# Kernel optimization log

Hardware: AMD Instinct MI355X
Metric: run time of the kernel (lower is better)

The kernel has to match this reference:

```python
import jax, jax.numpy as jnp
import numpy as np

N_NODES = 50000


def setup_inputs() -> dict:
    key = jax.random.key(0)
    k1, k2, k3, k4, k5, k6 = jax.random.split(key, 6)
    N, T, F_IN, F_OUT, E = N_NODES, 4, 64, 64, 800000
    node_features = jax.random.normal(k1, (N, T, F_IN), dtype=jnp.float32)
    edge_weights = jax.random.uniform(k2, (T, E), dtype=jnp.float32)
    src = jax.random.randint(k3, (E,), 0, N, dtype=jnp.int32)
    dst = jax.random.randint(k4, (E,), 0, N, dtype=jnp.int32)
    weight = jax.random.normal(k5, (F_OUT, F_IN), dtype=jnp.float32) / np.sqrt(F_IN)
    bias = jax.random.normal(k6, (F_OUT,), dtype=jnp.float32) * 0.01
    return {"node_features": node_features, "edge_weights": edge_weights,
            "src": src, "dst": dst, "weight": weight, "bias": bias}


def reference(node_features, edge_weights, src, dst, weight, bias):
    # edge_weights: (T, E) -> per-edge weights (E, T)
    ew = edge_weights.T  # (E, T)
    # gather source node features: (E, T, F); multiply by per-edge/timestep scalar
    msg = ew[:, :, None] * node_features[src]  # (E, T, F)
    # scatter-sum into destination nodes: (N, T, F)
    h = jax.ops.segment_sum(msg, dst, num_segments=N_NODES)
    # final linear: (N, T, F_out)
    out = jnp.einsum('ntf,of->nto', h, weight) + bias
    return out
```

## Files before the change

### kernel.cpp

```cpp
#include <hip/hip_runtime.h>


#define F_DIM 64
#define TF 256

typedef __attribute__((ext_vector_type(8))) short bf16x8;
typedef __attribute__((ext_vector_type(4))) float f32x4;
union frag_u { bf16x8 v; unsigned short s[8]; };

__device__ __forceinline__ unsigned short f2bf(float x) {
  unsigned u = __float_as_uint(x);
  return (unsigned short)((u + 0x7FFF + ((u >> 16) & 1)) >> 16);
}
__device__ __forceinline__ float bf2f(unsigned short b) {
  return __uint_as_float(((unsigned)b) << 16);
}

__global__ __launch_bounds__(256) void transform_hist_kernel(
    const float4* __restrict__ nf4, const float* __restrict__ W,
    unsigned short* __restrict__ nfb, int nrows,
    const int* __restrict__ dst, int* __restrict__ cnt, int E) {
  int lane = threadIdx.x & 63;
  int l15 = lane & 15, lg = lane >> 4;
  int wid = (blockIdx.x * 256 + threadIdx.x) >> 6;
  int nw = (gridDim.x * 256) >> 6;

  frag_u a[4][2];
  #pragma unroll
  for (int ot = 0; ot < 4; ++ot) {
    #pragma unroll
    for (int kh = 0; kh < 2; ++kh) {
      const float* wp = W + (ot * 16 + l15) * 64 + kh * 32 + lg * 8;
      float4 v0 = *reinterpret_cast<const float4*>(wp);
      float4 v1 = *reinterpret_cast<const float4*>(wp + 4);
      a[ot][kh].s[0] = f2bf(v0.x); a[ot][kh].s[1] = f2bf(v0.y);
      a[ot][kh].s[2] = f2bf(v0.z); a[ot][kh].s[3] = f2bf(v0.w);
      a[ot][kh].s[4] = f2bf(v1.x); a[ot][kh].s[5] = f2bf(v1.y);
      a[ot][kh].s[6] = f2bf(v1.z); a[ot][kh].s[7] = f2bf(v1.w);
    }
  }

  int ntiles = (nrows + 15) >> 4;
  for (int tile = wid; tile < ntiles; tile += nw) {
    int r = tile * 16 + l15;
    int rc = min(r, nrows - 1);
    const float4* bp = nf4 + (size_t)rc * 16 + lg * 2;
    float4 v0 = bp[0], v1 = bp[1];
    float4 v2 = bp[8], v3 = bp[9];
    frag_u b0, b1;
    b0.s[0] = f2bf(v0.x); b0.s[1] = f2bf(v0.y);
    b0.s[2] = f2bf(v0.z); b0.s[3] = f2bf(v0.w);
    b0.s[4] = f2bf(v1.x); b0.s[5] = f2bf(v1.y);
    b0.s[6] = f2bf(v1.z); b0.s[7] = f2bf(v1.w);
    b1.s[0] = f2bf(v2.x); b1.s[1] = f2bf(v2.y);
    b1.s[2] = f2bf(v2.z); b1.s[3] = f2bf(v2.w);
    b1.s[4] = f2bf(v3.x); b1.s[5] = f2bf(v3.y);
    b1.s[6] = f2bf(v3.z); b1.s[7] = f2bf(v3.w);

    f32x4 acc[4];
    #pragma unroll
    for (int ot = 0; ot < 4; ++ot) {
      f32x4 z = {0.f, 0.f, 0.f, 0.f};
      acc[ot] = __builtin_amdgcn_mfma_f32_16x16x32_bf16(a[ot][0].v, b0.v, z, 0, 0, 0);
      acc[ot] = __builtin_amdgcn_mfma_f32_16x16x32_bf16(a[ot][1].v, b1.v, acc[ot], 0, 0, 0);
    }
    if (r < nrows) {
      #pragma unroll
      for (int ot = 0; ot < 4; ++ot) {
        ushort4 u = make_ushort4(f2bf(acc[ot][0]), f2bf(acc[ot][1]),
                                 f2bf(acc[ot][2]), f2bf(acc[ot][3]));
        *reinterpret_cast<ushort4*>(
            &nfb[(size_t)r * F_DIM + ot * 16 + lg * 4]) = u;
      }
    }
  }

  int gtid = blockIdx.x * 256 + threadIdx.x;
  int gsz = gridDim.x * 256;
  for (int e = gtid; e < E; e += gsz) atomicAdd(&cnt[dst[e]], 1);
}

__global__ __launch_bounds__(1024) void scan_kernel(
    const int* __restrict__ cnt, int* __restrict__ off, int* __restrict__ bsum,
    int* __restrict__ sync, int N) {
  __shared__ int wsum[16];
  __shared__ int isLast;
  int tid = threadIdx.x;
  if (tid == 0) isLast = 0;
  int i = blockIdx.x * 1024 + tid;
  int v = (i < N) ? cnt[i] : 0;
  int lane = tid & 63;
  int incl = v;
  #pragma unroll
  for (int s = 1; s < 64; s <<= 1) {
    int t = __shfl_up(incl, s, 64);
    if (lane >= s) incl += t;
  }
  int w = tid >> 6;
  if (lane == 63) wsum[w] = incl;
  __syncthreads();
  if (w == 0) {
    int x = (lane < 16) ? wsum[lane] : 0;
    #pragma unroll
    for (int s = 1; s < 16; s <<= 1) {
      int t = __shfl_up(x, s, 64);
      if (lane >= s) x += t;
    }
    if (lane < 16) wsum[lane] = x;
  }
  __syncthreads();
  int wpre = (w == 0) ? 0 : wsum[w - 1];
  if (i < N) off[i] = wpre + incl - v;

  if (tid == 1023) {
    atomicExch(&bsum[blockIdx.x], wpre + incl);
    __threadfence();
    if (atomicAdd(sync, 1) == (int)gridDim.x - 1) isLast = 1;
  }
  __syncthreads();
  if (isLast && tid < 64) {
    int nb = gridDim.x;
    int bv = (tid < nb) ? atomicAdd(&bsum[tid], 0) : 0;
    int binc = bv;
    #pragma unroll
    for (int s = 1; s < 64; s <<= 1) {
      int t = __shfl_up(binc, s, 64);
      if (lane >= s) binc += t;
    }
    if (tid < nb) atomicExch(&bsum[tid], binc - bv);
  }
}

__global__ __launch_bounds__(256) void fill_kernel(
    const int* __restrict__ dst, const int* __restrict__ src,
    const float* __restrict__ ew, const int* __restrict__ off,
    const int* __restrict__ bsum, int* __restrict__ cnt,
    uint4* __restrict__ rec, int E) {
  int e = blockIdx.x * 256 + threadIdx.x;
  if (e < E) {
    int d = dst[e];
    int pos = off[d] + bsum[d >> 10] + atomicSub(&cnt[d], 1) - 1;
    unsigned w0 = f2bf(ew[e]),         w1 = f2bf(ew[E + e]);
    unsigned w2 = f2bf(ew[2 * E + e]), w3 = f2bf(ew[3 * E + e]);
    uint4 r;
    r.x = (unsigned)src[e];
    r.y = (w1 << 16) | w0;
    r.z = (w3 << 16) | w2;
    r.w = 0;
    rec[pos] = r;
  }
}

__global__ __launch_bounds__(256) void gather_bf16_kernel(
    const ushort4* __restrict__ nfb, const uint4* __restrict__ rec,
    const int* __restrict__ off, const int* __restrict__ bsum,
    const float4* __restrict__ bias4, float4* __restrict__ out4, int N, int E) {
  int idx = blockIdx.x * 256 + threadIdx.x;
  int n = idx >> 6;
  if (n >= N) return;
  n = __builtin_amdgcn_readfirstlane(n);
  int r = idx & 63, t = r >> 4, q = r & 15;
  int wsel = t >> 1;
  int wshift = (t & 1) << 4;
  int beg = off[n] + bsum[n >> 10];
  int end = (n + 1 < N) ? off[n + 1] + bsum[(n + 1) >> 10] : E;
  beg = __builtin_amdgcn_readfirstlane(beg);
  end = __builtin_amdgcn_readfirstlane(end);

  float4 acc = make_float4(0.f, 0.f, 0.f, 0.f);
  int p = beg;
  for (; p + 8 <= end; p += 8) {
    uint4 rr[8];
    #pragma unroll
    for (int j = 0; j < 8; ++j) rr[j] = rec[p + j];
    float w[8];
    ushort4 v[8];
    #pragma unroll
    for (int j = 0; j < 8; ++j) {
      w[j] = __uint_as_float(((wsel ? rr[j].z : rr[j].y) >> wshift) << 16);
      v[j] = nfb[(size_t)rr[j].x * 64 + t * 16 + q];
    }
    #pragma unroll
    for (int j = 0; j < 8; ++j) {
      acc.x += w[j] * bf2f(v[j].x);
      acc.y += w[j] * bf2f(v[j].y);
      acc.z += w[j] * bf2f(v[j].z);
      acc.w += w[j] * bf2f(v[j].w);
    }
  }
  for (; p + 4 <= end; p += 4) {
    uint4 rr[4];
    #pragma unroll
    for (int j = 0; j < 4; ++j) rr[j] = rec[p + j];
    #pragma unroll
    for (int j = 0; j < 4; ++j) {
      float w = __uint_as_float(((wsel ? rr[j].z : rr[j].y) >> wshift) << 16);
      ushort4 v = nfb[(size_t)rr[j].x * 64 + t * 16 + q];
      acc.x += w * bf2f(v.x); acc.y += w * bf2f(v.y);
      acc.z += w * bf2f(v.z); acc.w += w * bf2f(v.w);
    }
  }
  for (; p < end; ++p) {
    uint4 rr = rec[p];
    float w = __uint_as_float(((wsel ? rr.z : rr.y) >> wshift) << 16);
    ushort4 v = nfb[(size_t)rr.x * 64 + t * 16 + q];
    acc.x += w * bf2f(v.x); acc.y += w * bf2f(v.y);
    acc.z += w * bf2f(v.z); acc.w += w * bf2f(v.w);
  }
  float4 b = bias4[q];
  float4 res = make_float4(acc.x + b.x, acc.y + b.y, acc.z + b.z, acc.w + b.w);
  out4[(size_t)n * 64 + t * 16 + q] = res;
}

__global__ __launch_bounds__(256) void hist_kernel(
    const int* __restrict__ dst, int* __restrict__ cnt, int E) {
  int e = blockIdx.x * 256 + threadIdx.x;
  if (e < E) atomicAdd(&cnt[dst[e]], 1);
}

__global__ __launch_bounds__(256) void gather_f32_kernel(
    const float4* __restrict__ nf4, const uint4* __restrict__ rec,
    const int* __restrict__ off, const int* __restrict__ bsum,
    float4* __restrict__ h4, int N, int E) {
  int idx = blockIdx.x * 256 + threadIdx.x;
  int n = idx >> 6;
  if (n >= N) return;
  int r = idx & 63, t = r >> 4, q = r & 15;
  int wsel = t >> 1;
  int wshift = (t & 1) << 4;
  int beg = off[n] + bsum[n >> 10];
  int end = (n + 1 < N) ? off[n + 1] + bsum[(n + 1) >> 10] : E;
  float4 acc = make_float4(0.f, 0.f, 0.f, 0.f);
  for (int p = beg; p < end; ++p) {
    uint4 rr = rec[p];
    float w = __uint_as_float(((wsel ? rr.z : rr.y) >> wshift) << 16);
    float4 v = nf4[(size_t)rr.x * 64 + t * 16 + q];
    acc.x += w * v.x; acc.y += w * v.y; acc.z += w * v.z; acc.w += w * v.w;
  }
  h4[(size_t)n * 64 + t * 16 + q] = acc;
}

__global__ __launch_bounds__(256) void linear_kernel(
    float* __restrict__ h, const float* __restrict__ W,
    const float* __restrict__ bias, int nrows) {
  __shared__ float Wt[64 * 65];
  __shared__ float rows[4][64];
  int tid = threadIdx.x;
  for (int i = tid; i < 4096; i += 256) Wt[(i & 63) * 65 + (i >> 6)] = W[i];
  int rr = tid >> 6, o = tid & 63;
  float b = bias[o];
  int rbase = blockIdx.x * 32;
  for (int r0 = 0; r0 < 32; r0 += 4) {
    int row = rbase + r0 + rr;
    __syncthreads();
    if (row < nrows) rows[rr][o] = h[(size_t)row * F_DIM + o];
    __syncthreads();
    if (row < nrows) {
      float acc = b;
      #pragma unroll
      for (int f = 0; f < 64; ++f) acc += rows[rr][f] * Wt[f * 65 + o];
      h[(size_t)row * F_DIM + o] = acc;
    }
  }
}

extern "C" void kernel_launch(void* const* d_in, const int* in_sizes, int n_in,
                              void* d_out, int out_size, void* d_ws, size_t ws_size,
                              hipStream_t stream) {
  const float* nf   = (const float*)d_in[0];
  const float* ew   = (const float*)d_in[1];
  const int*   src  = (const int*)d_in[2];
  const int*   dst  = (const int*)d_in[3];
  const float* W    = (const float*)d_in[4];
  const float* bias = (const float*)d_in[5];
  float* out = (float*)d_out;

  int E = in_sizes[2];
  int N = out_size / TF;
  int nrows = out_size / F_DIM;
  int nfelems = nrows * F_DIM;

  char* wsb = (char*)d_ws;
  int* cnt  = (int*)wsb;
  int* sync = cnt + N;
  int* off  = sync + 1;
  int* bsum = off + (N + 1);
  size_t ofs = ((size_t)(2 * N + 2 + 64) * 4 + 15) & ~(size_t)15;
  uint4* rec = (uint4*)(wsb + ofs);           ofs += (size_t)E * 16;
  ofs = (ofs + 511) & ~(size_t)511;
  unsigned short* nfb = (unsigned short*)(wsb + ofs);
  size_t need_bf16 = ofs + (size_t)nfelems * 2;
  bool use_bf16 = ws_size >= need_bf16;

  (void)hipMemsetAsync(cnt, 0, (size_t)(N + 1) * sizeof(int), stream);

  int eblk = (E + 255) / 256;
  int sblk = (N + 1023) / 1024;

  if (use_bf16) {
    transform_hist_kernel<<<1024, 256, 0, stream>>>(
        (const float4*)nf, W, nfb, nrows, dst, cnt, E);
    scan_kernel<<<sblk, 1024, 0, stream>>>(cnt, off, bsum, sync, N);
    fill_kernel<<<eblk, 256, 0, stream>>>(dst, src, ew, off, bsum, cnt, rec, E);
    gather_bf16_kernel<<<(N * 64 + 255) / 256, 256, 0, stream>>>(
        (const ushort4*)nfb, rec, off, bsum, (const float4*)bias,
        (float4*)out, N, E);
  } else {
    hist_kernel<<<eblk, 256, 0, stream>>>(dst, cnt, E);
    scan_kernel<<<sblk, 1024, 0, stream>>>(cnt, off, bsum, sync, N);
    fill_kernel<<<eblk, 256, 0, stream>>>(dst, src, ew, off, bsum, cnt, rec, E);
    gather_f32_kernel<<<(N * 64 + 255) / 256, 256, 0, stream>>>(
        (const float4*)nf, rec, off, bsum, (float4*)out, N, E);
    linear_kernel<<<(nrows + 31) / 32, 256, 0, stream>>>(out, W, bias, nrows);
  }
}
```

Before: 161.8 us.

## Split bf16 gather into two timestep-pair passes with edge-parallel half-waves

The gather kernel now runs twice, each pass handling two of the four timesteps. Within a wave the two 32-lane halves process alternate edges and are combined at the end with a cross-lane shuffle. The aim is to shrink the working set of the random gathers per pass, so the bf16 node table slice for two timesteps fits better in cache, and to put more edges in flight per wave. The cost is reading the CSR records twice and launching an extra kernel. The transform kernel's grid is also doubled.

Result: slower. 367.4 us (+127.1%).

```diff
diff --git a/kernel.cpp b/kernel.cpp
--- a/kernel.cpp
+++ b/kernel.cpp
@@ -151,17 +151,21 @@
   }
 }
 
-__global__ __launch_bounds__(256) void gather_bf16_kernel(
+__global__ __launch_bounds__(256) void gather_tp_kernel(
     const ushort4* __restrict__ nfb, const uint4* __restrict__ rec,
     const int* __restrict__ off, const int* __restrict__ bsum,
-    const float4* __restrict__ bias4, float4* __restrict__ out4, int N, int E) {
+    const float4* __restrict__ bias4, float4* __restrict__ out4,
+    int N, int E, int tp) {
   int idx = blockIdx.x * 256 + threadIdx.x;
   int n = idx >> 6;
   if (n >= N) return;
   n = __builtin_amdgcn_readfirstlane(n);
-  int r = idx & 63, t = r >> 4, q = r & 15;
-  int wsel = t >> 1;
-  int wshift = (t & 1) << 4;
+  int lane = idx & 63;
+  int g = lane >> 5;
+  int tl = (lane >> 4) & 1;
+  int q = lane & 15;
+  int t = tp * 2 + tl;
+  int wshift = tl << 4;
   int beg = off[n] + bsum[n >> 10];
   int end = (n + 1 < N) ? off[n + 1] + bsum[(n + 1) >> 10] : E;
   beg = __builtin_amdgcn_readfirstlane(beg);
@@ -173,43 +177,50 @@
     uint4 rr[8];
     #pragma unroll
     for (int j = 0; j < 8; ++j) rr[j] = rec[p + j];
-    float w[8];
-    ushort4 v[8];
-    #pragma unroll
-    for (int j = 0; j < 8; ++j) {
-      w[j] = __uint_as_float(((wsel ? rr[j].z : rr[j].y) >> wshift) << 16);
-      v[j] = nfb[(size_t)rr[j].x * 64 + t * 16 + q];
-    }
-    #pragma unroll
-    for (int j = 0; j < 8; ++j) {
+    float w[4];
+    ushort4 v[4];
+    #pragma unroll
+    for (int j = 0; j < 4; ++j) {
+      uint4 rm = g ? rr[2 * j + 1] : rr[2 * j];
+      unsigned wp = tp ? rm.z : rm.y;
+      w[j] = __uint_as_float(((wp >> wshift) & 0xFFFFu) << 16);
+      v[j] = nfb[(size_t)rm.x * 64 + t * 16 + q];
+    }
+    #pragma unroll
+    for (int j = 0; j < 4; ++j) {
       acc.x += w[j] * bf2f(v[j].x);
       acc.y += w[j] * bf2f(v[j].y);
       acc.z += w[j] * bf2f(v[j].z);
       acc.w += w[j] * bf2f(v[j].w);
     }
   }
-  for (; p + 4 <= end; p += 4) {
-    uint4 rr[4];
-    #pragma unroll
-    for (int j = 0; j < 4; ++j) rr[j] = rec[p + j];
-    #pragma unroll
-    for (int j = 0; j < 4; ++j) {
-      float w = __uint_as_float(((wsel ? rr[j].z : rr[j].y) >> wshift) << 16);
-      ushort4 v = nfb[(size_t)rr[j].x * 64 + t * 16 + q];
-      acc.x += w * bf2f(v.x); acc.y += w * bf2f(v.y);
-      acc.z += w * bf2f(v.z); acc.w += w * bf2f(v.w);
-    }
-  }
-  for (; p < end; ++p) {
-    uint4 rr = rec[p];
-    float w = __uint_as_float(((wsel ? rr.z : rr.y) >> wshift) << 16);
-    ushort4 v = nfb[(size_t)rr.x * 64 + t * 16 + q];
+  for (; p + 2 <= end; p += 2) {
+    uint4 r0 = rec[p], r1 = rec[p + 1];
+    uint4 rm = g ? r1 : r0;
+    unsigned wp = tp ? rm.z : rm.y;
+    float w = __uint_as_float(((wp >> wshift) & 0xFFFFu) << 16);
+    ushort4 v = nfb[(size_t)rm.x * 64 + t * 16 + q];
     acc.x += w * bf2f(v.x); acc.y += w * bf2f(v.y);
     acc.z += w * bf2f(v.z); acc.w += w * bf2f(v.w);
   }
-  float4 b = bias4[q];
-  float4 res = make_float4(acc.x + b.x, acc.y + b.y, acc.z + b.z, acc.w + b.w);
-  out4[(size_t)n * 64 + t * 16 + q] = res;
+  if (p < end) {
+    uint4 rm = rec[p];
+    unsigned wp = tp ? rm.z : rm.y;
+    float w = __uint_as_float(((wp >> wshift) & 0xFFFFu) << 16);
+    if (g) w = 0.f;
+    ushort4 v = nfb[(size_t)rm.x * 64 + t * 16 + q];
+    acc.x += w * bf2f(v.x); acc.y += w * bf2f(v.y);
+    acc.z += w * bf2f(v.z); acc.w += w * bf2f(v.w);
+  }
+
+  acc.x += __shfl_xor(acc.x, 32); acc.y += __shfl_xor(acc.y, 32);
+  acc.z += __shfl_xor(acc.z, 32); acc.w += __shfl_xor(acc.w, 32);
+
+  if (g == 0) {
+    float4 b = bias4[q];
+    float4 res = make_float4(acc.x + b.x, acc.y + b.y, acc.z + b.z, acc.w + b.w);
+    out4[(size_t)n * 64 + t * 16 + q] = res;
+  }
 }
 
 __global__ __launch_bounds__(256) void hist_kernel(
@@ -296,20 +307,24 @@
 
   int eblk = (E + 255) / 256;
   int sblk = (N + 1023) / 1024;
+  int gblk = (N * 64 + 255) / 256;
 
   if (use_bf16) {
-    transform_hist_kernel<<<1024, 256, 0, stream>>>(
+    transform_hist_kernel<<<2048, 256, 0, stream>>>(
         (const float4*)nf, W, nfb, nrows, dst, cnt, E);
     scan_kernel<<<sblk, 1024, 0, stream>>>(cnt, off, bsum, sync, N);
     fill_kernel<<<eblk, 256, 0, stream>>>(dst, src, ew, off, bsum, cnt, rec, E);
-    gather_bf16_kernel<<<(N * 64 + 255) / 256, 256, 0, stream>>>(
+    gather_tp_kernel<<<gblk, 256, 0, stream>>>(
         (const ushort4*)nfb, rec, off, bsum, (const float4*)bias,
-        (float4*)out, N, E);
+        (float4*)out, N, E, 0);
+    gather_tp_kernel<<<gblk, 256, 0, stream>>>(
+        (const ushort4*)nfb, rec, off, bsum, (const float4*)bias,
+        (float4*)out, N, E, 1);
   } else {
     hist_kernel<<<eblk, 256, 0, stream>>>(dst, cnt, E);
     scan_kernel<<<sblk, 1024, 0, stream>>>(cnt, off, bsum, sync, N);
     fill_kernel<<<eblk, 256, 0, stream>>>(dst, src, ew, off, bsum, cnt, rec, E);
-    gather_f32_kernel<<<(N * 64 + 255) / 256, 256, 0, stream>>>(
+    gather_f32_kernel<<<gblk, 256, 0, stream>>>(
         (const float4*)nf, rec, off, bsum, (float4*)out, N, E);
     linear_kernel<<<(nrows + 31) / 32, 256, 0, stream>>>(out, W, bias, nrows);
   }
```
